# Optimization experiments

Hardware: AMD Instinct MI355X
Metric: run time of the kernel (lower is better)

The kernel has to match this reference:

```python
import jax, jax.numpy as jnp
import numpy as np

B, L, D, H = 4, 2048, 1024, 16
DH = D // H
SCALE = 1.0 / float(np.sqrt(DH))


def setup_inputs() -> dict:
    key = jax.random.key(0)
    ks = jax.random.split(key, 11)
    s = 0.02
    return {
        "q": jax.random.normal(ks[0], (B, L, D), jnp.float32),
        "k": jax.random.normal(ks[1], (B, L, D), jnp.float32),
        "v": jax.random.normal(ks[2], (B, L, D), jnp.float32),
        "Wq": jax.random.normal(ks[3], (D, D), jnp.float32) * s,
        "bq": jnp.zeros((D,), jnp.float32),
        "Wk": jax.random.normal(ks[4], (D, D), jnp.float32) * s,
        "bk": jnp.zeros((D,), jnp.float32),
        "Wv": jax.random.normal(ks[5], (D, D), jnp.float32) * s,
        "bv": jnp.zeros((D,), jnp.float32),
        "Wo": jax.random.normal(ks[6], (D, D), jnp.float32) * s,
        "bo": jnp.zeros((D,), jnp.float32),
    }


def _split_heads(x):
    # (B, L, D) -> (B, H, L, DH)
    b, l, _ = x.shape
    return x.reshape(b, l, H, DH).transpose(0, 2, 1, 3)


def reference(q, k, v, Wq, bq, Wk, bk, Wv, bv, Wo, bo):
    # torch Linear: y = x @ W.T + b
    qh = _split_heads(q @ Wq.T + bq)
    kh = _split_heads(k @ Wk.T + bk)
    vh = _split_heads(v @ Wv.T + bv)
    # Blocked loop in original == full attention: every q block sees all K/V.
    scores = jnp.einsum("bhqd,bhkd->bhqk", qh, kh) * SCALE
    attn = jax.nn.softmax(scores, axis=-1)  # dropout=0 (eval) -> identity
    out = jnp.einsum("bhqk,bhkd->bhqd", attn, vh)
    out = out.transpose(0, 2, 1, 3).reshape(q.shape[0], q.shape[1], D)
    return out @ Wo.T + bo
```

## Files before the change

### kernel.cpp

```cpp
#include <hip/hip_runtime.h>
#include <hip/hip_bf16.h>
#include <stdint.h>

#define NB  4
#define SEQ 2048
#define DIM 1024
#define NH  16
#define DHD 64
#define LOG2E 1.44269504088896340736f

typedef short short8 __attribute__((ext_vector_type(8)));
typedef float f32x4  __attribute__((ext_vector_type(4)));

__device__ __forceinline__ unsigned short f2bf(float f) {
  union { float f; uint32_t u; } x; x.f = f;
  uint32_t u = x.u;
  uint32_t r = (u + 0x7fffu + ((u >> 16) & 1u)) >> 16;
  return (unsigned short)r;
}

__device__ __forceinline__ uint32_t cvt_pk_bf16(float lo, float hi) {
  uint32_t r;
  asm("v_cvt_pk_bf16_f32 %0, %1, %2" : "=v"(r) : "v"(lo), "v"(hi));
  return r;
}

__device__ __forceinline__ void gload16(const void* g, void* l) {
  __builtin_amdgcn_global_load_lds(
      (const __attribute__((address_space(1))) uint32_t*)g,
      (__attribute__((address_space(3))) uint32_t*)l, 16, 0, 0);
}

__global__ void cvt_f32_bf16(const float* __restrict__ in,
                             unsigned short* __restrict__ out, int n4) {
  int i = blockIdx.x * blockDim.x + threadIdx.x;
  int stride = gridDim.x * blockDim.x;
  for (int j = i; j < n4; j += stride) {
    float4 v = reinterpret_cast<const float4*>(in)[j];
    ushort4 o;
    o.x = f2bf(v.x); o.y = f2bf(v.y); o.z = f2bf(v.z); o.w = f2bf(v.w);
    reinterpret_cast<ushort4*>(out)[j] = o;
  }
}

__global__ void cvt_w4(const float* __restrict__ w0, const float* __restrict__ w1,
                       const float* __restrict__ w2, const float* __restrict__ w3,
                       unsigned short* __restrict__ o0, unsigned short* __restrict__ o1,
                       unsigned short* __restrict__ o2, unsigned short* __restrict__ o3,
                       int n4) {
  int seg = blockIdx.x >> 8;
  int bid = blockIdx.x & 255;
  const float* in = (seg == 0) ? w0 : (seg == 1) ? w1 : (seg == 2) ? w2 : w3;
  unsigned short* out = (seg == 0) ? o0 : (seg == 1) ? o1 : (seg == 2) ? o2 : o3;
  for (int j = bid * 256 + threadIdx.x; j < n4; j += 65536) {
    float4 v = reinterpret_cast<const float4*>(in)[j];
    ushort4 o;
    o.x = f2bf(v.x); o.y = f2bf(v.y); o.z = f2bf(v.z); o.w = f2bf(v.w);
    reinterpret_cast<ushort4*>(out)[j] = o;
  }
}

template <int MODE, int AF32>
__global__ __launch_bounds__(256, 2) void gemm_bt(
    const unsigned short* __restrict__ A,
    const float* __restrict__ Af,
    const unsigned short* __restrict__ Bm,
    const float* __restrict__ bias,
    float* __restrict__ Cf,
    unsigned short* __restrict__ Cb,
    int M, int N, int K, float scale) {
  __shared__ uint4 smem[4096];

  const int tid  = threadIdx.x;
  const int lane = tid & 63;
  const int wid  = tid >> 6;
  const int cpx  = gridDim.x >> 3;
  const int wg   = (blockIdx.x & 7) * cpx + (blockIdx.x >> 3);
  const int nbn  = N >> 7;
  const int bm   = wg / nbn;
  const int bn   = wg % nbn;
  const int wrow = (wid >> 1) * 64;
  const int wcol = (wid & 1) * 64;

  f32x4 acc[4][4] = {};

  const unsigned short* pa[4];
  const float*          paf[4];
  const unsigned short* pb[4];
  uint4* la[4];
  uint4* lb[4];
#pragma unroll
  for (int i = 0; i < 4; ++i) {
    int c   = tid + (i << 8);
    int row = c >> 3;
    int kc  = (c & 7) ^ (row & 7);
    pa[i]  = A  + (size_t)(bm * 128 + row) * K + kc * 8;
    paf[i] = Af + (size_t)(bm * 128 + row) * K + kc * 8;
    pb[i]  = Bm + (size_t)(bn * 128 + row) * K + kc * 8;
    la[i] = smem + c;
    lb[i] = smem + 2048 + c;
  }

  float4 a32[4][2];
  auto loadA_f32 = [&](int kt) {
#pragma unroll
    for (int i = 0; i < 4; ++i) {
      a32[i][0] = *reinterpret_cast<const float4*>(paf[i] + kt * 64);
      a32[i][1] = *reinterpret_cast<const float4*>(paf[i] + kt * 64 + 4);
    }
  };
  auto writeA_bf16 = [&](int buf) {
#pragma unroll
    for (int i = 0; i < 4; ++i) {
      uint4 w;
      w.x = cvt_pk_bf16(a32[i][0].x, a32[i][0].y);
      w.y = cvt_pk_bf16(a32[i][0].z, a32[i][0].w);
      w.z = cvt_pk_bf16(a32[i][1].x, a32[i][1].y);
      w.w = cvt_pk_bf16(a32[i][1].z, a32[i][1].w);
      *(la[i] + buf * 1024) = w;
    }
  };
  auto stageA_g = [&](int kt, int buf) {
#pragma unroll
    for (int i = 0; i < 4; ++i) gload16(pa[i] + kt * 64, la[i] + buf * 1024);
  };
  auto stageB = [&](int kt, int buf) {
#pragma unroll
    for (int i = 0; i < 4; ++i) gload16(pb[i] + kt * 64, lb[i] + buf * 1024);
  };

  if (AF32) {
    loadA_f32(0);
    writeA_bf16(0);
  } else {
    stageA_g(0, 0);
  }
  stageB(0, 0);
  __syncthreads();

  const int NT = K >> 6;
  for (int kt = 0; kt < NT; ++kt) {
    const int cur = kt & 1;
    if (kt + 1 < NT) {
      if (AF32) loadA_f32(kt + 1);
      else      stageA_g(kt + 1, cur ^ 1);
      stageB(kt + 1, cur ^ 1);
    }

#pragma unroll
    for (int s = 0; s < 2; ++s) {
      short8 af[4], bfr[4];
#pragma unroll
      for (int mt = 0; mt < 4; ++mt) {
        int row = wrow + mt * 16 + (lane & 15);
        int ch  = ((s << 2) + (lane >> 4)) ^ (row & 7);
        af[mt]  = __builtin_bit_cast(short8, smem[cur * 1024 + row * 8 + ch]);
      }
#pragma unroll
      for (int nt = 0; nt < 4; ++nt) {
        int row = wcol + nt * 16 + (lane & 15);
        int ch  = ((s << 2) + (lane >> 4)) ^ (row & 7);
        bfr[nt] = __builtin_bit_cast(short8, smem[2048 + cur * 1024 + row * 8 + ch]);
      }
      __builtin_amdgcn_s_setprio(1);
#pragma unroll
      for (int mt = 0; mt < 4; ++mt)
#pragma unroll
        for (int nt = 0; nt < 4; ++nt)
          acc[mt][nt] = __builtin_amdgcn_mfma_f32_16x16x32_bf16(af[mt], bfr[nt], acc[mt][nt], 0, 0, 0);
      __builtin_amdgcn_s_setprio(0);
    }

    if (AF32 && kt + 1 < NT) writeA_bf16(cur ^ 1);
    __syncthreads();
  }

  const int rbase = bm * 128 + wrow + (lane >> 4) * 4;
  const int cbase = bn * 128 + wcol + (lane & 15);
#pragma unroll
  for (int nt = 0; nt < 4; ++nt) {
    int col  = cbase + nt * 16;
    float bv = bias[col];
#pragma unroll
    for (int mt = 0; mt < 4; ++mt) {
      if (MODE == 2) {
        int h = col >> 6, dh = col & 63;
        int row0 = rbase + mt * 16;
        int b = row0 >> 11, lq = row0 & 2047;
        uint2 pk;
        pk.x = cvt_pk_bf16((acc[mt][nt][0] + bv) * scale, (acc[mt][nt][1] + bv) * scale);
        pk.y = cvt_pk_bf16((acc[mt][nt][2] + bv) * scale, (acc[mt][nt][3] + bv) * scale);
        size_t dst = ((size_t)((b << 4) + h) * DHD + dh) * SEQ + lq;
        *reinterpret_cast<uint2*>(Cb + dst) = pk;
      } else {
#pragma unroll
        for (int r = 0; r < 4; ++r) {
          int row = rbase + mt * 16 + r;
          float v = acc[mt][nt][r] + bv;
          if (MODE == 0) {
            Cf[(size_t)row * N + col] = v;
          } else {
            v *= scale;
            int h = col >> 6, dh = col & 63;
            int b = row >> 11, lq = row & 2047;
            size_t dst = ((size_t)((b << 4) + h) * SEQ + lq) * DHD + dh;
            Cb[dst] = f2bf(v);
          }
        }
      }
    }
  }
}

__global__ __launch_bounds__(512, 4) void attn_kernel(
    const unsigned short* __restrict__ Qh,
    const unsigned short* __restrict__ Kh,
    const unsigned short* __restrict__ Vt,
    unsigned short* __restrict__ O) {
  __shared__ uint4 Kls[2][512];
  __shared__ uint4 Vls[2][512];
  __shared__ uint4 Pls[8][32 * 9];

  const int tid  = threadIdx.x;
  const int lane = tid & 63;
  const int wid  = tid >> 6;
  const int wg   = (blockIdx.x & 7) * 64 + (blockIdx.x >> 3);
  const int bh   = wg >> 3;
  const int qt   = wg & 7;
  const int qloc = lane & 15;
  const int grp  = lane >> 4;
  const int q7   = qloc & 7;

  const unsigned short* Qb = Qh + (size_t)bh * SEQ * DHD;
  const unsigned short* Kb = Kh + (size_t)bh * SEQ * DHD;
  const unsigned short* Vb = Vt + (size_t)bh * DHD * SEQ;

  const int srow = tid >> 3;
  const int skc  = (tid & 7) ^ (srow & 7);
  const unsigned short* pk0 = Kb + (size_t)srow * DHD + skc * 8;
  const unsigned short* pv0 = Vb + (size_t)srow * SEQ + skc * 8;
  auto stage = [&](int kt, int buf) {
    gload16(pk0 + (size_t)kt * 64 * DHD, &Kls[buf][tid]);
    gload16(pv0 + kt * 64,               &Vls[buf][tid]);
  };

  stage(0, 0);

  short8 qf[2][2];
#pragma unroll
  for (int qb = 0; qb < 2; ++qb) {
    int qrow = qt * 256 + wid * 32 + qb * 16 + qloc;
#pragma unroll
    for (int s = 0; s < 2; ++s)
      qf[qb][s] = *reinterpret_cast<const short8*>(Qb + (size_t)qrow * DHD + s * 32 + grp * 8);
  }

  const short8 ones = {0x3F80, 0x3F80, 0x3F80, 0x3F80, 0x3F80, 0x3F80, 0x3F80, 0x3F80};
  char* pwb = (char*)&Pls[wid][0];

  __syncthreads();

  float logbias = 0.f;
  f32x4 lsum[2] = {};
  f32x4 acc_o[4][2] = {};

  const int NT = SEQ / 64;
  for (int kt = 0; kt < NT; ++kt) {
    const int cur = kt & 1;
    if (kt + 1 < NT) stage(kt + 1, cur ^ 1);

    f32x4 sc[4][2];
    __builtin_amdgcn_s_setprio(1);
#pragma unroll
    for (int j = 0; j < 4; ++j) {
      short8 kf[2];
#pragma unroll
      for (int s = 0; s < 2; ++s) {
        int krow = j * 16 + qloc;
        int ch   = ((s << 2) + grp) ^ q7;
        kf[s] = __builtin_bit_cast(short8, Kls[cur][krow * 8 + ch]);
      }
#pragma unroll
      for (int qb = 0; qb < 2; ++qb) {
        f32x4 a = {logbias, logbias, logbias, logbias};
        a = __builtin_amdgcn_mfma_f32_16x16x32_bf16(kf[0], qf[qb][0], a, 0, 0, 0);
        a = __builtin_amdgcn_mfma_f32_16x16x32_bf16(kf[1], qf[qb][1], a, 0, 0, 0);
        sc[j][qb] = a;
      }
    }
    __builtin_amdgcn_s_setprio(0);

#pragma unroll
    for (int j = 0; j < 4; ++j)
#pragma unroll
      for (int qb = 0; qb < 2; ++qb) {
        float p0 = exp2f(sc[j][qb][0]);
        float p1 = exp2f(sc[j][qb][1]);
        float p2 = exp2f(sc[j][qb][2]);
        float p3 = exp2f(sc[j][qb][3]);
        uint2 w;
        w.x = cvt_pk_bf16(p0, p1);
        w.y = cvt_pk_bf16(p2, p3);
        *(uint2*)(pwb + (qb * 16 + qloc) * 144 + j * 32 + grp * 8) = w;
      }

    short8 pf[2][2];
#pragma unroll
    for (int qb = 0; qb < 2; ++qb)
#pragma unroll
      for (int t = 0; t < 2; ++t)
        pf[qb][t] = *(const short8*)(pwb + (qb * 16 + qloc) * 144 + t * 64 + grp * 16);

    __builtin_amdgcn_s_setprio(1);
#pragma unroll
    for (int db = 0; db < 4; ++db) {
      short8 vf[2];
#pragma unroll
      for (int t = 0; t < 2; ++t) {
        int vrow = db * 16 + qloc;
        int ch   = ((t << 2) + grp) ^ q7;
        vf[t] = __builtin_bit_cast(short8, Vls[cur][vrow * 8 + ch]);
      }
#pragma unroll
      for (int qb = 0; qb < 2; ++qb) {
        acc_o[db][qb] = __builtin_amdgcn_mfma_f32_16x16x32_bf16(vf[0], pf[qb][0], acc_o[db][qb], 0, 0, 0);
        acc_o[db][qb] = __builtin_amdgcn_mfma_f32_16x16x32_bf16(vf[1], pf[qb][1], acc_o[db][qb], 0, 0, 0);
      }
    }
#pragma unroll
    for (int qb = 0; qb < 2; ++qb) {
      lsum[qb] = __builtin_amdgcn_mfma_f32_16x16x32_bf16(ones, pf[qb][0], lsum[qb], 0, 0, 0);
      lsum[qb] = __builtin_amdgcn_mfma_f32_16x16x32_bf16(ones, pf[qb][1], lsum[qb], 0, 0, 0);
    }
    __builtin_amdgcn_s_setprio(0);

    if (__any(fmaxf(lsum[0][0], lsum[1][0]) > 7.9e28f)) {
      const float ds = 5.421010862e-20f;
      logbias -= 64.f;
#pragma unroll
      for (int db = 0; db < 4; ++db)
#pragma unroll
        for (int qb = 0; qb < 2; ++qb)
#pragma unroll
          for (int r = 0; r < 4; ++r) acc_o[db][qb][r] *= ds;
#pragma unroll
      for (int qb = 0; qb < 2; ++qb)
#pragma unroll
        for (int r = 0; r < 4; ++r) lsum[qb][r] *= ds;
    }

    __syncthreads();
  }

  const float inv0 = 1.0f / lsum[0][0];
  const float inv1 = 1.0f / lsum[1][0];
#pragma unroll
  for (int db = 0; db < 4; ++db)
#pragma unroll
    for (int qb = 0; qb < 2; ++qb) {
      float inv = qb ? inv1 : inv0;
      uint2 w;
      w.x = cvt_pk_bf16(acc_o[db][qb][0] * inv, acc_o[db][qb][1] * inv);
      w.y = cvt_pk_bf16(acc_o[db][qb][2] * inv, acc_o[db][qb][3] * inv);
      *(uint2*)(pwb + (qb * 16 + qloc) * 144 + db * 32 + grp * 8) = w;
    }
  const int b = bh >> 4, h = bh & 15;
#pragma unroll
  for (int pass = 0; pass < 4; ++pass) {
    int idx = pass * 64 + lane;
    int row = idx >> 3;
    int ck  = idx & 7;
    uint4 val = *(const uint4*)(pwb + row * 144 + ck * 16);
    int rowg  = qt * 256 + wid * 32 + row;
    *reinterpret_cast<uint4*>(O + ((size_t)(b * SEQ + rowg)) * DIM + (h << 6) + ck * 8) = val;
  }
}

extern "C" void kernel_launch(void* const* d_in, const int* in_sizes, int n_in,
                              void* d_out, int out_size, void* d_ws, size_t ws_size,
                              hipStream_t stream) {
  (void)in_sizes; (void)n_in; (void)out_size;
  const float* q  = (const float*)d_in[0];
  const float* k  = (const float*)d_in[1];
  const float* v  = (const float*)d_in[2];
  const float* Wq = (const float*)d_in[3];
  const float* bq = (const float*)d_in[4];
  const float* Wk = (const float*)d_in[5];
  const float* bk = (const float*)d_in[6];
  const float* Wv = (const float*)d_in[7];
  const float* bv = (const float*)d_in[8];
  const float* Wo = (const float*)d_in[9];
  const float* bo = (const float*)d_in[10];
  float* out = (float*)d_out;

  char* ws = (char*)d_ws;
  const size_t MB = 1024 * 1024;
  const int nW = DIM * DIM;
  const int M  = NB * SEQ;
  dim3 gg((M / 128) * (DIM / 128));
  const int attnGrid = NB * NH * (SEQ / 256);

  if (ws_size >= 73 * MB) {
    unsigned short* X   = (unsigned short*)(ws + 0);
    unsigned short* WXq = (unsigned short*)(ws + 16 * MB);
    unsigned short* WXk = (unsigned short*)(ws + 18 * MB);
    unsigned short* WXv = (unsigned short*)(ws + 20 * MB);
    unsigned short* WXo = (unsigned short*)(ws + 22 * MB);
    unsigned short* Qhp = (unsigned short*)(ws + 24 * MB);
    unsigned short* Khp = (unsigned short*)(ws + 40 * MB);
    unsigned short* Vtp = (unsigned short*)(ws + 56 * MB);

    cvt_w4<<<1024, 256, 0, stream>>>(Wq, Wk, Wv, Wo, WXq, WXk, WXv, WXo, nW / 4);
    gemm_bt<1, 1><<<gg, 256, 0, stream>>>(nullptr, q, WXq, bq, nullptr, Qhp, M, DIM, DIM, 0.125f * LOG2E);
    gemm_bt<1, 1><<<gg, 256, 0, stream>>>(nullptr, k, WXk, bk, nullptr, Khp, M, DIM, DIM, 1.0f);
    gemm_bt<2, 1><<<gg, 256, 0, stream>>>(nullptr, v, WXv, bv, nullptr, Vtp, M, DIM, DIM, 1.0f);
    attn_kernel<<<attnGrid, 512, 0, stream>>>(Qhp, Khp, Vtp, X);
    gemm_bt<0, 0><<<gg, 256, 0, stream>>>(X, nullptr, WXo, bo, out, nullptr, M, DIM, DIM, 1.0f);
  } else {
    unsigned short* X   = (unsigned short*)(ws + 0);
    unsigned short* WX  = (unsigned short*)(ws + 16 * MB);
    unsigned short* Qhp = (unsigned short*)(ws + 18 * MB);
    unsigned short* Khp = (unsigned short*)(ws + 34 * MB);
    unsigned short* Vtp = (unsigned short*)(ws + 50 * MB);

    cvt_f32_bf16<<<1024, 256, 0, stream>>>(Wq, WX, nW / 4);
    gemm_bt<1, 1><<<gg, 256, 0, stream>>>(nullptr, q, WX, bq, nullptr, Qhp, M, DIM, DIM, 0.125f * LOG2E);
    cvt_f32_bf16<<<1024, 256, 0, stream>>>(Wk, WX, nW / 4);
    gemm_bt<1, 1><<<gg, 256, 0, stream>>>(nullptr, k, WX, bk, nullptr, Khp, M, DIM, DIM, 1.0f);
    cvt_f32_bf16<<<1024, 256, 0, stream>>>(Wv, WX, nW / 4);
    gemm_bt<2, 1><<<gg, 256, 0, stream>>>(nullptr, v, WX, bv, nullptr, Vtp, M, DIM, DIM, 1.0f);
    attn_kernel<<<attnGrid, 512, 0, stream>>>(Qhp, Khp, Vtp, X);
    cvt_f32_bf16<<<1024, 256, 0, stream>>>(Wo, WX, nW / 4);
    gemm_bt<0, 0><<<gg, 256, 0, stream>>>(X, nullptr, WX, bo, out, nullptr, M, DIM, DIM, 1.0f);
  }
}
```

Baseline: 210.8 us.

## Merge Q/K/V projection GEMMs into one launch and interleave softmax with PV MFMAs

Replaces the three separate projection GEMM launches with a single 1536-workgroup kernel that picks the input, weight, bias and output layout from a segment index. This cuts two launches and their tail effects, and gives one larger grid for better CU fill. The attention inner loop now preloads all V fragments, then handles each query block in turn (exp, pack P, reload, PV and row-sum MFMAs) so exp work for one block can overlap MFMAs for the other. Holding all V fragments at once raises register pressure.

```diff
diff --git a/kernel.cpp b/kernel.cpp
--- a/kernel.cpp
+++ b/kernel.cpp
@@ -60,6 +60,144 @@
   }
 }
 
+__global__ __launch_bounds__(256, 2) void gemm_qkv(
+    const float* __restrict__ qs, const float* __restrict__ ks,
+    const float* __restrict__ vs,
+    const unsigned short* __restrict__ Wqb, const unsigned short* __restrict__ Wkb,
+    const unsigned short* __restrict__ Wvb,
+    const float* __restrict__ bqp, const float* __restrict__ bkp,
+    const float* __restrict__ bvp,
+    unsigned short* __restrict__ Qo, unsigned short* __restrict__ Ko,
+    unsigned short* __restrict__ Vo, float qscale) {
+  __shared__ uint4 smem[4096];
+
+  const int tid  = threadIdx.x;
+  const int lane = tid & 63;
+  const int wid  = tid >> 6;
+  const int wg   = (blockIdx.x & 7) * 192 + (blockIdx.x >> 3);
+  const int seg  = wg >> 9;
+  const int inner = wg & 511;
+  const float* Af = (seg == 0) ? qs : (seg == 1) ? ks : vs;
+  const unsigned short* Bm = (seg == 0) ? Wqb : (seg == 1) ? Wkb : Wvb;
+  const float* bias = (seg == 0) ? bqp : (seg == 1) ? bkp : bvp;
+  unsigned short* Cb = (seg == 0) ? Qo : (seg == 1) ? Ko : Vo;
+  const float scale = (seg == 0) ? qscale : 1.0f;
+  const int bm = inner >> 3;
+  const int bn = inner & 7;
+  const int wrow = (wid >> 1) * 64;
+  const int wcol = (wid & 1) * 64;
+  const int K = DIM;
+
+  f32x4 acc[4][4] = {};
+
+  const float*          paf[4];
+  const unsigned short* pb[4];
+  uint4* la[4];
+  uint4* lb[4];
+#pragma unroll
+  for (int i = 0; i < 4; ++i) {
+    int c   = tid + (i << 8);
+    int row = c >> 3;
+    int kc  = (c & 7) ^ (row & 7);
+    paf[i] = Af + (size_t)(bm * 128 + row) * K + kc * 8;
+    pb[i]  = Bm + (size_t)(bn * 128 + row) * K + kc * 8;
+    la[i] = smem + c;
+    lb[i] = smem + 2048 + c;
+  }
+
+  float4 a32[4][2];
+  auto loadA_f32 = [&](int kt) {
+#pragma unroll
+    for (int i = 0; i < 4; ++i) {
+      a32[i][0] = *reinterpret_cast<const float4*>(paf[i] + kt * 64);
+      a32[i][1] = *reinterpret_cast<const float4*>(paf[i] + kt * 64 + 4);
+    }
+  };
+  auto writeA_bf16 = [&](int buf) {
+#pragma unroll
+    for (int i = 0; i < 4; ++i) {
+      uint4 w;
+      w.x = cvt_pk_bf16(a32[i][0].x, a32[i][0].y);
+      w.y = cvt_pk_bf16(a32[i][0].z, a32[i][0].w);
+      w.z = cvt_pk_bf16(a32[i][1].x, a32[i][1].y);
+      w.w = cvt_pk_bf16(a32[i][1].z, a32[i][1].w);
+      *(la[i] + buf * 1024) = w;
+    }
+  };
+  auto stageB = [&](int kt, int buf) {
+#pragma unroll
+    for (int i = 0; i < 4; ++i) gload16(pb[i] + kt * 64, lb[i] + buf * 1024);
+  };
+
+  loadA_f32(0);
+  writeA_bf16(0);
+  stageB(0, 0);
+  __syncthreads();
+
+  const int NT = K >> 6;
+  for (int kt = 0; kt < NT; ++kt) {
+    const int cur = kt & 1;
+    if (kt + 1 < NT) {
+      loadA_f32(kt + 1);
+      stageB(kt + 1, cur ^ 1);
+    }
+
+#pragma unroll
+    for (int s = 0; s < 2; ++s) {
+      short8 af[4], bfr[4];
+#pragma unroll
+      for (int mt = 0; mt < 4; ++mt) {
+        int row = wrow + mt * 16 + (lane & 15);
+        int ch  = ((s << 2) + (lane >> 4)) ^ (row & 7);
+        af[mt]  = __builtin_bit_cast(short8, smem[cur * 1024 + row * 8 + ch]);
+      }
+#pragma unroll
+      for (int nt = 0; nt < 4; ++nt) {
+        int row = wcol + nt * 16 + (lane & 15);
+        int ch  = ((s << 2) + (lane >> 4)) ^ (row & 7);
+        bfr[nt] = __builtin_bit_cast(short8, smem[2048 + cur * 1024 + row * 8 + ch]);
+      }
+      __builtin_amdgcn_s_setprio(1);
+#pragma unroll
+      for (int mt = 0; mt < 4; ++mt)
+#pragma unroll
+        for (int nt = 0; nt < 4; ++nt)
+          acc[mt][nt] = __builtin_amdgcn_mfma_f32_16x16x32_bf16(af[mt], bfr[nt], acc[mt][nt], 0, 0, 0);
+      __builtin_amdgcn_s_setprio(0);
+    }
+
+    if (kt + 1 < NT) writeA_bf16(cur ^ 1);
+    __syncthreads();
+  }
+
+  const int rbase = bm * 128 + wrow + (lane >> 4) * 4;
+  const int cbase = bn * 128 + wcol + (lane & 15);
+#pragma unroll
+  for (int nt = 0; nt < 4; ++nt) {
+    int col  = cbase + nt * 16;
+    float bv = bias[col];
+    int h = col >> 6, dh = col & 63;
+#pragma unroll
+    for (int mt = 0; mt < 4; ++mt) {
+      if (seg == 2) {
+        int row0 = rbase + mt * 16;
+        int b = row0 >> 11, lq = row0 & 2047;
+        uint2 pk;
+        pk.x = cvt_pk_bf16(acc[mt][nt][0] + bv, acc[mt][nt][1] + bv);
+        pk.y = cvt_pk_bf16(acc[mt][nt][2] + bv, acc[mt][nt][3] + bv);
+        *reinterpret_cast<uint2*>(Cb + ((size_t)((b << 4) + h) * DHD + dh) * SEQ + lq) = pk;
+      } else {
+#pragma unroll
+        for (int r = 0; r < 4; ++r) {
+          int row = rbase + mt * 16 + r;
+          int b = row >> 11, lq = row & 2047;
+          Cb[((size_t)((b << 4) + h) * SEQ + lq) * DHD + dh] = f2bf((acc[mt][nt][r] + bv) * scale);
+        }
+      }
+    }
+  }
+}
+
 template <int MODE, int AF32>
 __global__ __launch_bounds__(256, 2) void gemm_bt(
     const unsigned short* __restrict__ A,
@@ -129,12 +267,8 @@
     for (int i = 0; i < 4; ++i) gload16(pb[i] + kt * 64, lb[i] + buf * 1024);
   };
 
-  if (AF32) {
-    loadA_f32(0);
-    writeA_bf16(0);
-  } else {
-    stageA_g(0, 0);
-  }
+  if (AF32) { loadA_f32(0); writeA_bf16(0); }
+  else      { stageA_g(0, 0); }
   stageB(0, 0);
   __syncthreads();
 
@@ -190,8 +324,7 @@
         uint2 pk;
         pk.x = cvt_pk_bf16((acc[mt][nt][0] + bv) * scale, (acc[mt][nt][1] + bv) * scale);
         pk.y = cvt_pk_bf16((acc[mt][nt][2] + bv) * scale, (acc[mt][nt][3] + bv) * scale);
-        size_t dst = ((size_t)((b << 4) + h) * DHD + dh) * SEQ + lq;
-        *reinterpret_cast<uint2*>(Cb + dst) = pk;
+        *reinterpret_cast<uint2*>(Cb + ((size_t)((b << 4) + h) * DHD + dh) * SEQ + lq) = pk;
       } else {
 #pragma unroll
         for (int r = 0; r < 4; ++r) {
@@ -203,8 +336,7 @@
             v *= scale;
             int h = col >> 6, dh = col & 63;
             int b = row >> 11, lq = row & 2047;
-            size_t dst = ((size_t)((b << 4) + h) * SEQ + lq) * DHD + dh;
-            Cb[dst] = f2bf(v);
+            Cb[((size_t)((b << 4) + h) * SEQ + lq) * DHD + dh] = f2bf(v);
           }
         }
       }
@@ -290,49 +422,37 @@
     }
     __builtin_amdgcn_s_setprio(0);
 
-#pragma unroll
-    for (int j = 0; j < 4; ++j)
-#pragma unroll
-      for (int qb = 0; qb < 2; ++qb) {
-        float p0 = exp2f(sc[j][qb][0]);
-        float p1 = exp2f(sc[j][qb][1]);
-        float p2 = exp2f(sc[j][qb][2]);
-        float p3 = exp2f(sc[j][qb][3]);
-        uint2 w;
-        w.x = cvt_pk_bf16(p0, p1);
-        w.y = cvt_pk_bf16(p2, p3);
-        *(uint2*)(pwb + (qb * 16 + qloc) * 144 + j * 32 + grp * 8) = w;
-      }
-
-    short8 pf[2][2];
-#pragma unroll
-    for (int qb = 0; qb < 2; ++qb)
-#pragma unroll
-      for (int t = 0; t < 2; ++t)
-        pf[qb][t] = *(const short8*)(pwb + (qb * 16 + qloc) * 144 + t * 64 + grp * 16);
-
-    __builtin_amdgcn_s_setprio(1);
-#pragma unroll
-    for (int db = 0; db < 4; ++db) {
-      short8 vf[2];
+    short8 vf[4][2];
+#pragma unroll
+    for (int db = 0; db < 4; ++db)
 #pragma unroll
       for (int t = 0; t < 2; ++t) {
         int vrow = db * 16 + qloc;
         int ch   = ((t << 2) + grp) ^ q7;
-        vf[t] = __builtin_bit_cast(short8, Vls[cur][vrow * 8 + ch]);
-      }
-#pragma unroll
-      for (int qb = 0; qb < 2; ++qb) {
-        acc_o[db][qb] = __builtin_amdgcn_mfma_f32_16x16x32_bf16(vf[0], pf[qb][0], acc_o[db][qb], 0, 0, 0);
-        acc_o[db][qb] = __builtin_amdgcn_mfma_f32_16x16x32_bf16(vf[1], pf[qb][1], acc_o[db][qb], 0, 0, 0);
-      }
-    }
+        vf[db][t] = __builtin_bit_cast(short8, Vls[cur][vrow * 8 + ch]);
+      }
+
 #pragma unroll
     for (int qb = 0; qb < 2; ++qb) {
-      lsum[qb] = __builtin_amdgcn_mfma_f32_16x16x32_bf16(ones, pf[qb][0], lsum[qb], 0, 0, 0);
-      lsum[qb] = __builtin_amdgcn_mfma_f32_16x16x32_bf16(ones, pf[qb][1], lsum[qb], 0, 0, 0);
-    }
-    __builtin_amdgcn_s_setprio(0);
+#pragma unroll
+      for (int j = 0; j < 4; ++j) {
+        uint2 w;
+        w.x = cvt_pk_bf16(exp2f(sc[j][qb][0]), exp2f(sc[j][qb][1]));
+        w.y = cvt_pk_bf16(exp2f(sc[j][qb][2]), exp2f(sc[j][qb][3]));
+        *(uint2*)(pwb + (qb * 16 + qloc) * 144 + j * 32 + grp * 8) = w;
+      }
+      short8 pf0 = *(const short8*)(pwb + (qb * 16 + qloc) * 144 + 0 * 64 + grp * 16);
+      short8 pf1 = *(const short8*)(pwb + (qb * 16 + qloc) * 144 + 1 * 64 + grp * 16);
+      __builtin_amdgcn_s_setprio(1);
+#pragma unroll
+      for (int db = 0; db < 4; ++db) {
+        acc_o[db][qb] = __builtin_amdgcn_mfma_f32_16x16x32_bf16(vf[db][0], pf0, acc_o[db][qb], 0, 0, 0);
+        acc_o[db][qb] = __builtin_amdgcn_mfma_f32_16x16x32_bf16(vf[db][1], pf1, acc_o[db][qb], 0, 0, 0);
+      }
+      lsum[qb] = __builtin_amdgcn_mfma_f32_16x16x32_bf16(ones, pf0, lsum[qb], 0, 0, 0);
+      lsum[qb] = __builtin_amdgcn_mfma_f32_16x16x32_bf16(ones, pf1, lsum[qb], 0, 0, 0);
+      __builtin_amdgcn_s_setprio(0);
+    }
 
     if (__any(fmaxf(lsum[0][0], lsum[1][0]) > 7.9e28f)) {
       const float ds = 5.421010862e-20f;
@@ -411,9 +531,8 @@
     unsigned short* Vtp = (unsigned short*)(ws + 56 * MB);
 
     cvt_w4<<<1024, 256, 0, stream>>>(Wq, Wk, Wv, Wo, WXq, WXk, WXv, WXo, nW / 4);
-    gemm_bt<1, 1><<<gg, 256, 0, stream>>>(nullptr, q, WXq, bq, nullptr, Qhp, M, DIM, DIM, 0.125f * LOG2E);
-    gemm_bt<1, 1><<<gg, 256, 0, stream>>>(nullptr, k, WXk, bk, nullptr, Khp, M, DIM, DIM, 1.0f);
-    gemm_bt<2, 1><<<gg, 256, 0, stream>>>(nullptr, v, WXv, bv, nullptr, Vtp, M, DIM, DIM, 1.0f);
+    gemm_qkv<<<1536, 256, 0, stream>>>(q, k, v, WXq, WXk, WXv, bq, bk, bv,
+                                       Qhp, Khp, Vtp, 0.125f * LOG2E);
     attn_kernel<<<attnGrid, 512, 0, stream>>>(Qhp, Khp, Vtp, X);
     gemm_bt<0, 0><<<gg, 256, 0, stream>>>(X, nullptr, WXo, bo, out, nullptr, M, DIM, DIM, 1.0f);
   } else {
```

Result: slower. 236.2 us (+12.0%).

## Permute K rows at staging so P stays in registers, skipping LDS round-trip

Applied to the files above, without the earlier changes.

K tile rows are loaded into LDS in a permuted order, so the S=K·Q^T MFMA output registers already match the B-operand layout the P·V MFMA expects. The exp2/bf16 results are then packed straight into short8 operands, with no write to per-wave LDS and no read back. This removes LDS stores, loads and their latency from each KV iteration. V fragments are also loaded up front and the PV MFMAs are interleaved per query block, which raises register pressure.

```diff
diff --git a/kernel.cpp b/kernel.cpp
--- a/kernel.cpp
+++ b/kernel.cpp
@@ -129,12 +129,8 @@
     for (int i = 0; i < 4; ++i) gload16(pb[i] + kt * 64, lb[i] + buf * 1024);
   };
 
-  if (AF32) {
-    loadA_f32(0);
-    writeA_bf16(0);
-  } else {
-    stageA_g(0, 0);
-  }
+  if (AF32) { loadA_f32(0); writeA_bf16(0); }
+  else      { stageA_g(0, 0); }
   stageB(0, 0);
   __syncthreads();
 
@@ -190,8 +186,7 @@
         uint2 pk;
         pk.x = cvt_pk_bf16((acc[mt][nt][0] + bv) * scale, (acc[mt][nt][1] + bv) * scale);
         pk.y = cvt_pk_bf16((acc[mt][nt][2] + bv) * scale, (acc[mt][nt][3] + bv) * scale);
-        size_t dst = ((size_t)((b << 4) + h) * DHD + dh) * SEQ + lq;
-        *reinterpret_cast<uint2*>(Cb + dst) = pk;
+        *reinterpret_cast<uint2*>(Cb + ((size_t)((b << 4) + h) * DHD + dh) * SEQ + lq) = pk;
       } else {
 #pragma unroll
         for (int r = 0; r < 4; ++r) {
@@ -203,8 +198,7 @@
             v *= scale;
             int h = col >> 6, dh = col & 63;
             int b = row >> 11, lq = row & 2047;
-            size_t dst = ((size_t)((b << 4) + h) * SEQ + lq) * DHD + dh;
-            Cb[dst] = f2bf(v);
+            Cb[((size_t)((b << 4) + h) * SEQ + lq) * DHD + dh] = f2bf(v);
           }
         }
       }
@@ -237,7 +231,9 @@
 
   const int srow = tid >> 3;
   const int skc  = (tid & 7) ^ (srow & 7);
-  const unsigned short* pk0 = Kb + (size_t)srow * DHD + skc * 8;
+  const int krow_g = ((srow >> 5) << 5) | (((srow >> 2) & 3) << 3)
+                   | (((srow >> 4) & 1) << 2) | (srow & 3);
+  const unsigned short* pk0 = Kb + (size_t)krow_g * DHD + skc * 8;
   const unsigned short* pv0 = Vb + (size_t)srow * SEQ + skc * 8;
   auto stage = [&](int kt, int buf) {
     gload16(pk0 + (size_t)kt * 64 * DHD, &Kls[buf][tid]);
@@ -290,49 +286,39 @@
     }
     __builtin_amdgcn_s_setprio(0);
 
-#pragma unroll
-    for (int j = 0; j < 4; ++j)
-#pragma unroll
-      for (int qb = 0; qb < 2; ++qb) {
-        float p0 = exp2f(sc[j][qb][0]);
-        float p1 = exp2f(sc[j][qb][1]);
-        float p2 = exp2f(sc[j][qb][2]);
-        float p3 = exp2f(sc[j][qb][3]);
-        uint2 w;
-        w.x = cvt_pk_bf16(p0, p1);
-        w.y = cvt_pk_bf16(p2, p3);
-        *(uint2*)(pwb + (qb * 16 + qloc) * 144 + j * 32 + grp * 8) = w;
-      }
-
-    short8 pf[2][2];
-#pragma unroll
-    for (int qb = 0; qb < 2; ++qb)
-#pragma unroll
-      for (int t = 0; t < 2; ++t)
-        pf[qb][t] = *(const short8*)(pwb + (qb * 16 + qloc) * 144 + t * 64 + grp * 16);
-
-    __builtin_amdgcn_s_setprio(1);
-#pragma unroll
-    for (int db = 0; db < 4; ++db) {
-      short8 vf[2];
+    short8 vf[4][2];
+#pragma unroll
+    for (int db = 0; db < 4; ++db)
 #pragma unroll
       for (int t = 0; t < 2; ++t) {
         int vrow = db * 16 + qloc;
         int ch   = ((t << 2) + grp) ^ q7;
-        vf[t] = __builtin_bit_cast(short8, Vls[cur][vrow * 8 + ch]);
-      }
-#pragma unroll
-      for (int qb = 0; qb < 2; ++qb) {
-        acc_o[db][qb] = __builtin_amdgcn_mfma_f32_16x16x32_bf16(vf[0], pf[qb][0], acc_o[db][qb], 0, 0, 0);
-        acc_o[db][qb] = __builtin_amdgcn_mfma_f32_16x16x32_bf16(vf[1], pf[qb][1], acc_o[db][qb], 0, 0, 0);
-      }
-    }
+        vf[db][t] = __builtin_bit_cast(short8, Vls[cur][vrow * 8 + ch]);
+      }
+
 #pragma unroll
     for (int qb = 0; qb < 2; ++qb) {
-      lsum[qb] = __builtin_amdgcn_mfma_f32_16x16x32_bf16(ones, pf[qb][0], lsum[qb], 0, 0, 0);
-      lsum[qb] = __builtin_amdgcn_mfma_f32_16x16x32_bf16(ones, pf[qb][1], lsum[qb], 0, 0, 0);
-    }
-    __builtin_amdgcn_s_setprio(0);
+      uint4 p0, p1;
+      p0.x = cvt_pk_bf16(exp2f(sc[0][qb][0]), exp2f(sc[0][qb][1]));
+      p0.y = cvt_pk_bf16(exp2f(sc[0][qb][2]), exp2f(sc[0][qb][3]));
+      p0.z = cvt_pk_bf16(exp2f(sc[1][qb][0]), exp2f(sc[1][qb][1]));
+      p0.w = cvt_pk_bf16(exp2f(sc[1][qb][2]), exp2f(sc[1][qb][3]));
+      p1.x = cvt_pk_bf16(exp2f(sc[2][qb][0]), exp2f(sc[2][qb][1]));
+      p1.y = cvt_pk_bf16(exp2f(sc[2][qb][2]), exp2f(sc[2][qb][3]));
+      p1.z = cvt_pk_bf16(exp2f(sc[3][qb][0]), exp2f(sc[3][qb][1]));
+      p1.w = cvt_pk_bf16(exp2f(sc[3][qb][2]), exp2f(sc[3][qb][3]));
+      short8 pf0 = __builtin_bit_cast(short8, p0);
+      short8 pf1 = __builtin_bit_cast(short8, p1);
+      __builtin_amdgcn_s_setprio(1);
+#pragma unroll
+      for (int db = 0; db < 4; ++db) {
+        acc_o[db][qb] = __builtin_amdgcn_mfma_f32_16x16x32_bf16(vf[db][0], pf0, acc_o[db][qb], 0, 0, 0);
+        acc_o[db][qb] = __builtin_amdgcn_mfma_f32_16x16x32_bf16(vf[db][1], pf1, acc_o[db][qb], 0, 0, 0);
+      }
+      lsum[qb] = __builtin_amdgcn_mfma_f32_16x16x32_bf16(ones, pf0, lsum[qb], 0, 0, 0);
+      lsum[qb] = __builtin_amdgcn_mfma_f32_16x16x32_bf16(ones, pf1, lsum[qb], 0, 0, 0);
+      __builtin_amdgcn_s_setprio(0);
+    }
 
     if (__any(fmaxf(lsum[0][0], lsum[1][0]) > 7.9e28f)) {
       const float ds = 5.421010862e-20f;
```

Result: slower. 228.6 us (+8.4%).
